# Performance work log

Hardware: AMD Instinct MI355X
Metric: run time of the kernel (lower is better)

The kernel has to match this reference:

```python
import jax, jax.numpy as jnp
import numpy as np
import math

EMBED = 1024
HEADS = 16
HEAD_DIM = EMBED // HEADS
FFN = 4 * EMBED
LAYERS = 3
SEQ = 2048
BATCH = 2
INPUT_DIM = 64


def make_pe(max_len, d_model):
    pe = np.zeros((max_len, d_model), dtype=np.float32)
    pos = np.arange(max_len, dtype=np.float32)[:, None]
    div = np.exp(np.arange(0, d_model, 2, dtype=np.float32) * (-math.log(10000.0) / d_model))
    pe[:, 0::2] = np.sin(pos * div)
    pe[:, 1::2] = np.cos(pos * div)
    return jnp.asarray(pe)


def setup_inputs() -> dict:
    key = jax.random.key(0)
    ks = jax.random.split(key, 16)
    s = lambda k, shape, fan: jax.random.normal(k, shape, dtype=jnp.float32) / np.sqrt(fan)
    return {
        "x": jax.random.normal(ks[0], (BATCH, SEQ, INPUT_DIM), dtype=jnp.float32),
        "mask": jnp.ones((BATCH, 1, 1, SEQ), dtype=bool),
        "embed_W": s(ks[1], (INPUT_DIM, EMBED), INPUT_DIM),
        "embed_b": jnp.zeros((EMBED,), jnp.float32),
        "pe": make_pe(SEQ, EMBED),
        "Wq": s(ks[2], (LAYERS, HEAD_DIM, HEAD_DIM), HEAD_DIM),
        "Wk": s(ks[3], (LAYERS, HEAD_DIM, HEAD_DIM), HEAD_DIM),
        "Wv": s(ks[4], (LAYERS, HEAD_DIM, HEAD_DIM), HEAD_DIM),
        "Wo": s(ks[5], (LAYERS, EMBED, EMBED), EMBED),
        "bo": jnp.zeros((LAYERS, EMBED), jnp.float32),
        "ln1_g": jnp.ones((LAYERS, EMBED), jnp.float32),
        "ln1_b": jnp.zeros((LAYERS, EMBED), jnp.float32),
        "W1": s(ks[6], (LAYERS, EMBED, FFN), EMBED),
        "b1": jnp.zeros((LAYERS, FFN), jnp.float32),
        "W2": s(ks[7], (LAYERS, FFN, EMBED), FFN),
        "b2": jnp.zeros((LAYERS, EMBED), jnp.float32),
        "ln2_g": jnp.ones((LAYERS, EMBED), jnp.float32),
        "ln2_b": jnp.zeros((LAYERS, EMBED), jnp.float32),
    }


def _layernorm(x, g, b, eps=1e-5):
    mu = jnp.mean(x, axis=-1, keepdims=True)
    var = jnp.var(x, axis=-1, keepdims=True)
    return (x - mu) * jax.lax.rsqrt(var + eps) * g + b


def reference(x, mask, embed_W, embed_b, pe, Wq, Wk, Wv, Wo, bo,
              ln1_g, ln1_b, W1, b1, W2, b2, ln2_g, ln2_b):
    N, S, _ = x.shape
    scale = 1.0 / np.sqrt(EMBED).astype(np.float32)  # note: sqrt(embed_size), as in original
    h = x @ embed_W + embed_b + pe[None, :S, :]
    for l in range(LAYERS):
        hr = h.reshape(N, S, HEADS, HEAD_DIM)
        q = jnp.einsum('nshd,de->nshe', hr, Wq[l])
        k = jnp.einsum('nshd,de->nshe', hr, Wk[l])
        v = jnp.einsum('nshd,de->nshe', hr, Wv[l])
        energy = jnp.einsum('nqhd,nkhd->nhqk', q, k)  # (N,H,S,S)
        energy = jnp.where(mask == 0, jnp.float32(-1e20), energy)
        attn = jax.nn.softmax(energy * scale, axis=-1)
        o = jnp.einsum('nhqk,nkhd->nqhd', attn, v).reshape(N, S, EMBED)
        o = o @ Wo[l] + bo[l]
        x1 = _layernorm(o + h, ln1_g[l], ln1_b[l])
        ff = jax.nn.relu(x1 @ W1[l] + b1[l]) @ W2[l] + b2[l]
        h = _layernorm(ff + x1, ln2_g[l], ln2_b[l])
    return h
```

## Files before the change

kernel.cpp:

```cpp
#include <hip/hip_runtime.h>


typedef __attribute__((ext_vector_type(8))) unsigned short us8;
typedef __attribute__((ext_vector_type(4))) unsigned short us4;
typedef __attribute__((ext_vector_type(8))) __bf16 bf16x8;
typedef __attribute__((ext_vector_type(4))) float f32x4;

#define SEQ   2048
#define HEADS 16
#define HD    64
#define EMB   1024
#define FFN_  4096
#define NBAT  2
#define ROWS  (NBAT*SEQ)

__device__ __forceinline__ float bf2f(unsigned short s) {
    return __builtin_bit_cast(float, ((unsigned int)s) << 16);
}
__device__ __forceinline__ unsigned short f2bf(float f) {
    unsigned int u = __builtin_bit_cast(unsigned int, f);
    u += 0x7fffu + ((u >> 16) & 1u);
    return (unsigned short)(u >> 16);
}
__device__ __forceinline__ bf16x8 ldfrag(const unsigned short* p) {
    us8 v = *(const us8*)p;
    return __builtin_bit_cast(bf16x8, v);
}
__device__ __forceinline__ us8 cvt8(const float* p) {
    float4 f0 = *(const float4*)p, f1 = *(const float4*)(p + 4);
    us8 v;
    v[0] = f2bf(f0.x); v[1] = f2bf(f0.y); v[2] = f2bf(f0.z); v[3] = f2bf(f0.w);
    v[4] = f2bf(f1.x); v[5] = f2bf(f1.y); v[6] = f2bf(f1.z); v[7] = f2bf(f1.w);
    return v;
}
__device__ __forceinline__ void async_cp16(const unsigned short* g, unsigned short* l) {
    __builtin_amdgcn_global_load_lds(
        (const __attribute__((address_space(1))) void*)g,
        (__attribute__((address_space(3))) void*)l, 16, 0, 0);
}

__device__ __forceinline__ void transpose_tile(
    const float* __restrict__ W, unsigned short* __restrict__ Wt,
    int K, int N, int k0, int n0, int t)
{
    __shared__ float T[64][65];
    const int kk = t >> 4, nn = (t & 15) * 4;
#pragma unroll
    for (int r = 0; r < 4; r++) {
        float4 v = *(const float4*)(W + (size_t)(k0 + kk + r*16)*N + n0 + nn);
        T[kk + r*16][nn+0] = v.x; T[kk + r*16][nn+1] = v.y;
        T[kk + r*16][nn+2] = v.z; T[kk + r*16][nn+3] = v.w;
    }
    __syncthreads();
    const int n = t >> 2, kc = (t & 3) * 16;
    us8 a, b;
#pragma unroll
    for (int i = 0; i < 8; i++) a[i] = f2bf(T[kc + i][n]);
#pragma unroll
    for (int i = 0; i < 8; i++) b[i] = f2bf(T[kc + 8 + i][n]);
    *(us8*)(Wt + (size_t)(n0 + n)*K + k0 + kc)     = a;
    *(us8*)(Wt + (size_t)(n0 + n)*K + k0 + kc + 8) = b;
}

__global__ __launch_bounds__(256) void wprep(
    const float* __restrict__ W, unsigned short* __restrict__ Wt,
    const int K, const int N)
{
    transpose_tile(W, Wt, K, N, blockIdx.x*64, blockIdx.y*64, threadIdx.x);
}

__global__ __launch_bounds__(256) void wprep_qkv(
    const float* __restrict__ Wq, const float* __restrict__ Wk,
    const float* __restrict__ Wv, unsigned short* __restrict__ Wt3)
{
    const float* W = blockIdx.z == 0 ? Wq : (blockIdx.z == 1 ? Wk : Wv);
    transpose_tile(W, Wt3 + (size_t)blockIdx.z*64*64, 64, 64, 0, 0, threadIdx.x);
}

__global__ __launch_bounds__(256) void cvt_bf16(
    const float* __restrict__ src, unsigned short* __restrict__ dst, const int n8)
{
    int i = blockIdx.x*256 + threadIdx.x;
    if (i < n8) *(us8*)(dst + (size_t)i*8) = cvt8(src + (size_t)i*8);
}

__global__ __launch_bounds__(256) void vtrans(
    const unsigned short* __restrict__ QKV, unsigned short* __restrict__ Vt)
{
    __shared__ __align__(16) unsigned short T[64*72];
    const int s0 = blockIdx.x*64, h = blockIdx.y, n = blockIdx.z;
    const int t = threadIdx.x;
    const int s = t & 63, c16 = (t >> 6) * 16;
    const unsigned short* src =
        QKV + ((size_t)(n*SEQ + s0 + s)*HEADS + h)*192 + 128 + c16;
    *(us8*)&T[s*72 + c16]     = *(const us8*)(src);
    *(us8*)&T[s*72 + c16 + 8] = *(const us8*)(src + 8);
    __syncthreads();
    const int f = t & 63, r16 = (t >> 6) * 16;
    us8 a, b;
#pragma unroll
    for (int i = 0; i < 8; i++) a[i] = T[(r16 + i)*72 + f];
#pragma unroll
    for (int i = 0; i < 8; i++) b[i] = T[(r16 + 8 + i)*72 + f];
    unsigned short* dst = Vt + ((size_t)(n*HEADS + h)*HD + f)*SEQ + s0 + r16;
    *(us8*)dst       = a;
    *(us8*)(dst + 8) = b;
}

template<int BM, int BN, int WR, int WC>
__global__ __launch_bounds__(WR*WC*64) void gemm_bt(
    const unsigned short* __restrict__ A, const unsigned short* __restrict__ Bt,
    void* __restrict__ Cout, const int out_bf16,
    const float* __restrict__ bias, const float* __restrict__ pe,
    const int M, const int N, const int K, const int relu)
{
    constexpr int BK  = 32;
    constexpr int NW  = WR*WC;
    constexpr int ACH = BM*4;
    constexpr int BCH = BN*4;
    constexpr int APW = ACH/NW;
    constexpr int BPW = BCH/NW;
    __shared__ __align__(16) unsigned short As[BM*BK];
    __shared__ __align__(16) unsigned short Bs[BN*BK];

    const int tid  = threadIdx.x;
    const int lane = tid & 63;
    const int wave = tid >> 6;
    const int wm   = (wave / WC) * 64;
    const int wn   = (wave % WC) * 64;
    const int bm   = blockIdx.x * BM;
    const int bn   = blockIdx.y * BN;
    const int m15  = lane & 15;
    const int quad = lane >> 4;

    f32x4 acc[4][4];
#pragma unroll
    for (int i = 0; i < 4; i++)
#pragma unroll
        for (int j = 0; j < 4; j++) acc[i][j] = (f32x4){0.f, 0.f, 0.f, 0.f};

    for (int kt = 0; kt < K; kt += BK) {
#pragma unroll
        for (int j = 0; j < APW/64; j++) {
            const int c = wave*APW + j*64 + lane;
            async_cp16(A + (size_t)(bm + (c >> 2))*K + kt + (c & 3)*8,
                       As + (size_t)(wave*APW + j*64)*8);
        }
#pragma unroll
        for (int j = 0; j < BPW/64; j++) {
            const int c = wave*BPW + j*64 + lane;
            async_cp16(Bt + (size_t)(bn + (c >> 2))*K + kt + (c & 3)*8,
                       Bs + (size_t)(wave*BPW + j*64)*8);
        }
        __syncthreads();

        bf16x8 af[4], bfr[4];
#pragma unroll
        for (int i = 0; i < 4; i++) af[i]  = ldfrag(&As[(wm + i*16 + m15)*BK + quad*8]);
#pragma unroll
        for (int j = 0; j < 4; j++) bfr[j] = ldfrag(&Bs[(wn + j*16 + m15)*BK + quad*8]);
#pragma unroll
        for (int i = 0; i < 4; i++)
#pragma unroll
            for (int j = 0; j < 4; j++)
                acc[i][j] = __builtin_amdgcn_mfma_f32_16x16x32_bf16(af[i], bfr[j], acc[i][j], 0, 0, 0);
        __syncthreads();
    }

#pragma unroll
    for (int i = 0; i < 4; i++) {
#pragma unroll
        for (int j = 0; j < 4; j++) {
#pragma unroll
            for (int r = 0; r < 4; r++) {
                int row = bm + wm + i*16 + quad*4 + r;
                int col = bn + wn + j*16 + m15;
                float v = acc[i][j][r];
                if (bias) v += bias[col];
                if (pe)   v += pe[(size_t)(row & (SEQ-1))*EMB + col];
                if (relu) v = fmaxf(v, 0.f);
                if (out_bf16) ((unsigned short*)Cout)[(size_t)row*N + col] = f2bf(v);
                else          ((float*)Cout)[(size_t)row*N + col] = v;
            }
        }
    }
}

__global__ __launch_bounds__(256, 2) void flash_attn(
    const unsigned short* __restrict__ QKV, const unsigned short* __restrict__ Vt,
    unsigned short* __restrict__ O)
{
    const int h = blockIdx.y, n = blockIdx.z;
    const int tid = threadIdx.x, lane = tid & 63, wave = tid >> 6;
    const int m15 = lane & 15, quad = lane >> 4;
    const int q0 = blockIdx.x*128 + wave*32;

    __shared__ __align__(16) unsigned short Pl[4][32*36];

    bf16x8 aq[2][2];
#pragma unroll
    for (int mi = 0; mi < 2; mi++) {
        const unsigned short* qp =
            QKV + ((size_t)(n*SEQ + q0 + mi*16 + m15)*HEADS + h)*192;
        aq[mi][0] = ldfrag(qp + quad*8);
        aq[mi][1] = ldfrag(qp + 32 + quad*8);
    }

    f32x4 accO[2][4];
    f32x4 lacc[2];
#pragma unroll
    for (int mi = 0; mi < 2; mi++) {
        lacc[mi] = (f32x4){0.f, 0.f, 0.f, 0.f};
#pragma unroll
        for (int ft = 0; ft < 4; ft++) accO[mi][ft] = (f32x4){0.f, 0.f, 0.f, 0.f};
    }

    const float sl2e = 0.03125f * 1.4426950408889634f;
    const unsigned short* kb = QKV + ((size_t)(n*SEQ)*HEADS + h)*192 + 64;
    const unsigned short* vb = Vt + (size_t)(n*HEADS + h)*HD*SEQ;

    us8 ones_u;
#pragma unroll
    for (int i = 0; i < 8; i++) ones_u[i] = 0x3F80;
    const bf16x8 ones = __builtin_bit_cast(bf16x8, ones_u);

    auto load_kv = [&](bf16x8 (&dk)[2][2], bf16x8 (&dv)[4], int kt) {
#pragma unroll
        for (int nt = 0; nt < 2; nt++)
#pragma unroll
            for (int ks = 0; ks < 2; ks++)
                dk[nt][ks] = ldfrag(kb + (size_t)(kt + nt*16 + m15)*(HEADS*192)
                                       + ks*32 + quad*8);
#pragma unroll
        for (int ft = 0; ft < 4; ft++)
            dv[ft] = ldfrag(vb + (size_t)(ft*16 + m15)*SEQ + kt + quad*8);
    };

    auto step = [&](bf16x8 (&ck)[2][2], bf16x8 (&cv)[4],
                    bf16x8 (&nk)[2][2], bf16x8 (&nv)[4], int ktn) {
        load_kv(nk, nv, ktn);

        f32x4 sv[2][2];
        __builtin_amdgcn_s_setprio(1);
#pragma unroll
        for (int mi = 0; mi < 2; mi++)
#pragma unroll
            for (int nt = 0; nt < 2; nt++) {
                f32x4 z = (f32x4){0.f, 0.f, 0.f, 0.f};
                z = __builtin_amdgcn_mfma_f32_16x16x32_bf16(aq[mi][0], ck[nt][0], z, 0, 0, 0);
                z = __builtin_amdgcn_mfma_f32_16x16x32_bf16(aq[mi][1], ck[nt][1], z, 0, 0, 0);
                sv[mi][nt] = z;
            }
        __builtin_amdgcn_s_setprio(0);

#pragma unroll
        for (int mi = 0; mi < 2; mi++)
#pragma unroll
            for (int nt = 0; nt < 2; nt++)
#pragma unroll
                for (int r = 0; r < 4; r++) {
                    float p = exp2f(fminf(sv[mi][nt][r] * sl2e, 80.f));
                    Pl[wave][(mi*16 + quad*4 + r)*36 + nt*16 + m15] = f2bf(p);
                }

        bf16x8 pf[2];
#pragma unroll
        for (int mi = 0; mi < 2; mi++)
            pf[mi] = ldfrag(&Pl[wave][(mi*16 + m15)*36 + quad*8]);
        __builtin_amdgcn_s_setprio(1);
#pragma unroll
        for (int mi = 0; mi < 2; mi++) {
#pragma unroll
            for (int ft = 0; ft < 4; ft++)
                accO[mi][ft] = __builtin_amdgcn_mfma_f32_16x16x32_bf16(
                    pf[mi], cv[ft], accO[mi][ft], 0, 0, 0);
            lacc[mi] = __builtin_amdgcn_mfma_f32_16x16x32_bf16(
                pf[mi], ones, lacc[mi], 0, 0, 0);
        }
        __builtin_amdgcn_s_setprio(0);
    };

    bf16x8 k0[2][2], v0[4], k1[2][2], v1[4];
    load_kv(k0, v0, 0);
    for (int kt = 0; kt < SEQ; kt += 64) {
        step(k0, v0, k1, v1, kt + 32);
        step(k1, v1, k0, v0, (kt + 64) & (SEQ - 1));
    }

#pragma unroll
    for (int mi = 0; mi < 2; mi++)
#pragma unroll
        for (int r = 0; r < 4; r++) {
            const float inv = 1.0f / lacc[mi][r];
            const int row = q0 + mi*16 + quad*4 + r;
#pragma unroll
            for (int ft = 0; ft < 4; ft++)
                O[((size_t)(n*SEQ + row)*HEADS + h)*HD + ft*16 + m15] =
                    f2bf(accO[mi][ft][r] * inv);
        }
}

__global__ __launch_bounds__(256) void add_ln_kernel(
    const unsigned short* __restrict__ a, const unsigned short* __restrict__ res,
    const float* __restrict__ g, const float* __restrict__ b,
    void* __restrict__ out, const int out_fp32)
{
    const int row = blockIdx.x;
    const int tid = threadIdx.x;
    const int c0  = tid * 4;

    us4 va = *(const us4*)(a   + (size_t)row*EMB + c0);
    us4 vr = *(const us4*)(res + (size_t)row*EMB + c0);
    float x[4];
#pragma unroll
    for (int i = 0; i < 4; i++) x[i] = bf2f(va[i]) + bf2f(vr[i]);

    float s = x[0] + x[1] + x[2] + x[3];
    float q = x[0]*x[0] + x[1]*x[1] + x[2]*x[2] + x[3]*x[3];
#pragma unroll
    for (int off = 1; off < 64; off <<= 1) {
        s += __shfl_xor(s, off, 64);
        q += __shfl_xor(q, off, 64);
    }
    __shared__ float rs[4], rq[4];
    if ((tid & 63) == 0) { rs[tid >> 6] = s; rq[tid >> 6] = q; }
    __syncthreads();
    s = rs[0] + rs[1] + rs[2] + rs[3];
    q = rq[0] + rq[1] + rq[2] + rq[3];

    const float mu   = s * (1.0f/EMB);
    const float var  = q * (1.0f/EMB) - mu*mu;
    const float rstd = rsqrtf(var + 1e-5f);

    float4 vg = *(const float4*)(g + c0);
    float4 vb = *(const float4*)(b + c0);
    float y0 = (x[0] - mu) * rstd * vg.x + vb.x;
    float y1 = (x[1] - mu) * rstd * vg.y + vb.y;
    float y2 = (x[2] - mu) * rstd * vg.z + vb.z;
    float y3 = (x[3] - mu) * rstd * vg.w + vb.w;

    if (out_fp32) {
        *(float4*)((float*)out + (size_t)row*EMB + c0) = (float4){y0, y1, y2, y3};
    } else {
        us4 o;
        o[0] = f2bf(y0); o[1] = f2bf(y1); o[2] = f2bf(y2); o[3] = f2bf(y3);
        *(us4*)((unsigned short*)out + (size_t)row*EMB + c0) = o;
    }
}

extern "C" void kernel_launch(void* const* d_in, const int* in_sizes, int n_in,
                              void* d_out, int out_size, void* d_ws, size_t ws_size,
                              hipStream_t stream)
{
    (void)in_sizes; (void)n_in; (void)out_size; (void)ws_size;
    const float* x    = (const float*)d_in[0];
    const float* embW = (const float*)d_in[2];
    const float* embB = (const float*)d_in[3];
    const float* pe   = (const float*)d_in[4];
    const float* Wq   = (const float*)d_in[5];
    const float* Wk   = (const float*)d_in[6];
    const float* Wv   = (const float*)d_in[7];
    const float* Wo   = (const float*)d_in[8];
    const float* bo   = (const float*)d_in[9];
    const float* ln1g = (const float*)d_in[10];
    const float* ln1b = (const float*)d_in[11];
    const float* W1   = (const float*)d_in[12];
    const float* b1   = (const float*)d_in[13];
    const float* W2   = (const float*)d_in[14];
    const float* b2   = (const float*)d_in[15];
    const float* ln2g = (const float*)d_in[16];
    const float* ln2b = (const float*)d_in[17];

    char* ws = (char*)d_ws;
    const size_t MB = 1024*1024;
    unsigned short* qkv = (unsigned short*)ws;
    unsigned short* ff  = (unsigned short*)ws;
    unsigned short* vt  = (unsigned short*)(ws + 24*MB);
    unsigned short* t   = (unsigned short*)(ws + 32*MB);
    unsigned short* h   = (unsigned short*)(ws + 40*MB);
    unsigned short* x1  = (unsigned short*)(ws + 48*MB);
    unsigned short* wx  = (unsigned short*)(ws + 56*MB);
    unsigned short* xb    = t;
    unsigned short* embWt = t + 256*1024;
    unsigned short* qkvWt = t;
    unsigned short* o   = (unsigned short*)d_out;

    cvt_bf16<<<128, 256, 0, stream>>>(x, xb, ROWS*64/8);
    wprep<<<dim3(1, EMB/64), 256, 0, stream>>>(embW, embWt, 64, EMB);
    gemm_bt<128,128,2,2><<<dim3(ROWS/128, EMB/128), 256, 0, stream>>>(
        xb, embWt, h, 1, embB, pe, ROWS, EMB, 64, 0);

    for (int l = 0; l < 3; l++) {
        wprep_qkv<<<dim3(1,1,3), 256, 0, stream>>>(
            Wq + (size_t)l*HD*HD, Wk + (size_t)l*HD*HD, Wv + (size_t)l*HD*HD, qkvWt);
        gemm_bt<256,64,4,1><<<dim3(ROWS*HEADS/256, 3), 256, 0, stream>>>(
            h, qkvWt, qkv, 1, nullptr, nullptr, ROWS*HEADS, 192, HD, 0);

        vtrans<<<dim3(SEQ/64, HEADS, NBAT), 256, 0, stream>>>(qkv, vt);
        flash_attn<<<dim3(SEQ/128, HEADS, NBAT), 256, 0, stream>>>(qkv, vt, o);

        wprep<<<dim3(EMB/64, EMB/64), 256, 0, stream>>>(
            Wo + (size_t)l*EMB*EMB, wx, EMB, EMB);
        gemm_bt<128,128,2,2><<<dim3(ROWS/128, EMB/128), 256, 0, stream>>>(
            o, wx, t, 1, bo + (size_t)l*EMB, nullptr, ROWS, EMB, EMB, 0);
        add_ln_kernel<<<ROWS, 256, 0, stream>>>(
            t, h, ln1g + (size_t)l*EMB, ln1b + (size_t)l*EMB, x1, 0);

        wprep<<<dim3(EMB/64, FFN_/64), 256, 0, stream>>>(
            W1 + (size_t)l*EMB*FFN_, wx, EMB, FFN_);
        gemm_bt<128,128,2,2><<<dim3(ROWS/128, FFN_/128), 256, 0, stream>>>(
            x1, wx, ff, 1, b1 + (size_t)l*FFN_, nullptr, ROWS, FFN_, EMB, 1);
        wprep<<<dim3(FFN_/64, EMB/64), 256, 0, stream>>>(
            W2 + (size_t)l*FFN_*EMB, wx, FFN_, EMB);
        gemm_bt<128,128,2,2><<<dim3(ROWS/128, EMB/128), 256, 0, stream>>>(
            ff, wx, t, 1, b2 + (size_t)l*EMB, nullptr, ROWS, EMB, FFN_, 0);

        if (l == 2)
            add_ln_kernel<<<ROWS, 256, 0, stream>>>(
                t, x1, ln2g + (size_t)l*EMB, ln2b + (size_t)l*EMB, d_out, 1);
        else
            add_ln_kernel<<<ROWS, 256, 0, stream>>>(
                t, x1, ln2g + (size_t)l*EMB, ln2b + (size_t)l*EMB, h, 0);
    }
}
```

Measured before the change: 1.330 ms.

## Stage K/V tiles in shared memory via async copies in flash attention

Replaces the per-wave direct global loads of K and V fragments (register double-buffered) with block-cooperative async 16-byte copies into swizzled shared-memory tiles of 64 keys, shared by all four waves. This is meant to cut redundant global/L2 traffic, since every wave previously loaded the same K/V data itself. The cost is two block barriers per tile and the loss of the load/compute overlap that register prefetching gave, since loads are no longer double-buffered. Launch bounds also drop the two-blocks-per-SM hint.

```diff
diff --git a/kernel.cpp b/kernel.cpp
--- a/kernel.cpp
+++ b/kernel.cpp
@@ -186,7 +186,7 @@
     }
 }
 
-__global__ __launch_bounds__(256, 2) void flash_attn(
+__global__ __launch_bounds__(256) void flash_attn(
     const unsigned short* __restrict__ QKV, const unsigned short* __restrict__ Vt,
     unsigned short* __restrict__ O)
 {
@@ -195,6 +195,8 @@
     const int m15 = lane & 15, quad = lane >> 4;
     const int q0 = blockIdx.x*128 + wave*32;
 
+    __shared__ __align__(16) unsigned short Ks[64*64];
+    __shared__ __align__(16) unsigned short Vs[64*64];
     __shared__ __align__(16) unsigned short Pl[4][32*36];
 
     bf16x8 aq[2][2];
@@ -224,67 +226,74 @@
     for (int i = 0; i < 8; i++) ones_u[i] = 0x3F80;
     const bf16x8 ones = __builtin_bit_cast(bf16x8, ones_u);
 
-    auto load_kv = [&](bf16x8 (&dk)[2][2], bf16x8 (&dv)[4], int kt) {
-#pragma unroll
-        for (int nt = 0; nt < 2; nt++)
-#pragma unroll
-            for (int ks = 0; ks < 2; ks++)
-                dk[nt][ks] = ldfrag(kb + (size_t)(kt + nt*16 + m15)*(HEADS*192)
-                                       + ks*32 + quad*8);
-#pragma unroll
-        for (int ft = 0; ft < 4; ft++)
-            dv[ft] = ldfrag(vb + (size_t)(ft*16 + m15)*SEQ + kt + quad*8);
-    };
-
-    auto step = [&](bf16x8 (&ck)[2][2], bf16x8 (&cv)[4],
-                    bf16x8 (&nk)[2][2], bf16x8 (&nv)[4], int ktn) {
-        load_kv(nk, nv, ktn);
-
-        f32x4 sv[2][2];
-        __builtin_amdgcn_s_setprio(1);
-#pragma unroll
-        for (int mi = 0; mi < 2; mi++)
-#pragma unroll
-            for (int nt = 0; nt < 2; nt++) {
-                f32x4 z = (f32x4){0.f, 0.f, 0.f, 0.f};
-                z = __builtin_amdgcn_mfma_f32_16x16x32_bf16(aq[mi][0], ck[nt][0], z, 0, 0, 0);
-                z = __builtin_amdgcn_mfma_f32_16x16x32_bf16(aq[mi][1], ck[nt][1], z, 0, 0, 0);
-                sv[mi][nt] = z;
+    const int r0  = tid >> 3;
+    const int r1  = r0 + 32;
+    const int sc  = ((tid & 7) ^ (r0 & 7)) * 8;
+    const int swz = (m15 & 7);
+
+    for (int kt = 0; kt < SEQ; kt += 64) {
+        async_cp16(kb + (size_t)(kt + r0)*(HEADS*192) + sc, Ks + (size_t)(wave*64)*8);
+        async_cp16(kb + (size_t)(kt + r1)*(HEADS*192) + sc, Ks + (size_t)(256 + wave*64)*8);
+        async_cp16(vb + (size_t)r0*SEQ + kt + sc,           Vs + (size_t)(wave*64)*8);
+        async_cp16(vb + (size_t)r1*SEQ + kt + sc,           Vs + (size_t)(256 + wave*64)*8);
+        __syncthreads();
+
+#pragma unroll
+        for (int s2 = 0; s2 < 2; s2++) {
+            bf16x8 ck[2][2], cv[4];
+#pragma unroll
+            for (int nt = 0; nt < 2; nt++)
+#pragma unroll
+                for (int ks = 0; ks < 2; ks++) {
+                    const int kk = s2*32 + nt*16 + m15;
+                    ck[nt][ks] = ldfrag(&Ks[kk*64 + (((ks*4 + quad) ^ swz) * 8)]);
+                }
+#pragma unroll
+            for (int ft = 0; ft < 4; ft++) {
+                const int d = ft*16 + m15;
+                cv[ft] = ldfrag(&Vs[d*64 + (((s2*4 + quad) ^ swz) * 8)]);
             }
-        __builtin_amdgcn_s_setprio(0);
-
-#pragma unroll
-        for (int mi = 0; mi < 2; mi++)
-#pragma unroll
-            for (int nt = 0; nt < 2; nt++)
-#pragma unroll
-                for (int r = 0; r < 4; r++) {
-                    float p = exp2f(fminf(sv[mi][nt][r] * sl2e, 80.f));
-                    Pl[wave][(mi*16 + quad*4 + r)*36 + nt*16 + m15] = f2bf(p);
+
+            f32x4 sv[2][2];
+            __builtin_amdgcn_s_setprio(1);
+#pragma unroll
+            for (int mi = 0; mi < 2; mi++)
+#pragma unroll
+                for (int nt = 0; nt < 2; nt++) {
+                    f32x4 z = (f32x4){0.f, 0.f, 0.f, 0.f};
+                    z = __builtin_amdgcn_mfma_f32_16x16x32_bf16(aq[mi][0], ck[nt][0], z, 0, 0, 0);
+                    z = __builtin_amdgcn_mfma_f32_16x16x32_bf16(aq[mi][1], ck[nt][1], z, 0, 0, 0);
+                    sv[mi][nt] = z;
                 }
-
-        bf16x8 pf[2];
-#pragma unroll
-        for (int mi = 0; mi < 2; mi++)
-            pf[mi] = ldfrag(&Pl[wave][(mi*16 + m15)*36 + quad*8]);
-        __builtin_amdgcn_s_setprio(1);
-#pragma unroll
-        for (int mi = 0; mi < 2; mi++) {
-#pragma unroll
-            for (int ft = 0; ft < 4; ft++)
-                accO[mi][ft] = __builtin_amdgcn_mfma_f32_16x16x32_bf16(
-                    pf[mi], cv[ft], accO[mi][ft], 0, 0, 0);
-            lacc[mi] = __builtin_amdgcn_mfma_f32_16x16x32_bf16(
-                pf[mi], ones, lacc[mi], 0, 0, 0);
+            __builtin_amdgcn_s_setprio(0);
+
+#pragma unroll
+            for (int mi = 0; mi < 2; mi++)
+#pragma unroll
+                for (int nt = 0; nt < 2; nt++)
+#pragma unroll
+                    for (int r = 0; r < 4; r++) {
+                        float p = exp2f(fminf(sv[mi][nt][r] * sl2e, 80.f));
+                        Pl[wave][(mi*16 + quad*4 + r)*36 + nt*16 + m15] = f2bf(p);
+                    }
+
+            bf16x8 pf[2];
+#pragma unroll
+            for (int mi = 0; mi < 2; mi++)
+                pf[mi] = ldfrag(&Pl[wave][(mi*16 + m15)*36 + quad*8]);
+            __builtin_amdgcn_s_setprio(1);
+#pragma unroll
+            for (int mi = 0; mi < 2; mi++) {
+#pragma unroll
+                for (int ft = 0; ft < 4; ft++)
+                    accO[mi][ft] = __builtin_amdgcn_mfma_f32_16x16x32_bf16(
+                        pf[mi], cv[ft], accO[mi][ft], 0, 0, 0);
+                lacc[mi] = __builtin_amdgcn_mfma_f32_16x16x32_bf16(
+                    pf[mi], ones, lacc[mi], 0, 0, 0);
+            }
+            __builtin_amdgcn_s_setprio(0);
         }
-        __builtin_amdgcn_s_setprio(0);
-    };
-
-    bf16x8 k0[2][2], v0[4], k1[2][2], v1[4];
-    load_kv(k0, v0, 0);
-    for (int kt = 0; kt < SEQ; kt += 64) {
-        step(k0, v0, k1, v1, kt + 32);
-        step(k1, v1, k0, v0, (kt + 64) & (SEQ - 1));
+        __syncthreads();
     }
 
 #pragma unroll
```

Result: faster. 1.256 ms (-5.6%).
